# Optimization experiments

Measured on AMD Instinct MI355X. Metric: run time of the kernel, lower is better.

## Reference

```python
import jax, jax.numpy as jnp
import numpy as np


def setup_inputs() -> dict:
    key = jax.random.key(0)
    k1, k2, k3 = jax.random.split(key, 3)
    B, Cin, H, W = 64, 16, 256, 256
    Cout, K = 64, 3
    x = jax.random.normal(k1, (B, Cin, H, W), dtype=jnp.float32)
    # PyTorch Conv2d init scale ~ 1/sqrt(fan_in)
    fan_in = Cin * K * K
    conv_weight = jax.random.normal(k2, (Cout, Cin, K, K), dtype=jnp.float32) / np.sqrt(fan_in)
    conv_bias = jax.random.normal(k3, (Cout,), dtype=jnp.float32) / np.sqrt(fan_in)
    return {"x": x, "conv_weight": conv_weight, "conv_bias": conv_bias}


def reference(x, conv_weight, conv_bias):
    # Conv2d: stride=1, padding=0 (VALID), dilation=1, groups=1
    y = jax.lax.conv_general_dilated(
        x, conv_weight,
        window_strides=(1, 1),
        padding="VALID",
        dimension_numbers=("NCHW", "OIHW", "NCHW"),
    ) + conv_bias[None, :, None, None]          # [B, Cout, 254, 254]
    m = jnp.min(y, axis=1, keepdims=True)        # [B, 1, 254, 254] min over channels
    return jnp.tanh(jnp.tanh(m))                 # double tanh
```

## Files before the change

### kernel.cpp

```cpp
#include <hip/hip_runtime.h>
#include <math.h>

#define CIN   16
#define COUT  64
#define H     256
#define W     256
#define OH    254
#define OW    254
#define NTAP  9
#define HWSZ  (H * W)
#define TOR   8
#define TIR   10
#define SROW  264
#define BUFS  (TIR * SROW)
#define NTILE 16

typedef _Float16 f16x8  __attribute__((ext_vector_type(8)));
typedef float    f32x16 __attribute__((ext_vector_type(16)));

__global__ void wpack_kernel(const float* __restrict__ w, _Float16* __restrict__ wpk) {
    int idx = blockIdx.x * 256 + threadIdx.x;
    if (idx >= NTAP * 2 * 64 * 8) return;
    int e = idx & 7, l = (idx >> 3) & 63, m = (idx >> 9) & 1, t = idx >> 10;
    int co  = (l & 31) + 32 * m;
    int cin = 8 * (l >> 5) + e;
    wpk[idx] = (_Float16)w[((co * CIN + cin) * 3 + t / 3) * 3 + (t % 3)];
}

__device__ __forceinline__ float tanh_fast(float v) {
    float e = __expf(2.0f * v);
    return 1.0f - 2.0f * __builtin_amdgcn_rcpf(e + 1.0f);
}
__device__ __forceinline__ float min3f(float a, float b, float c) {
    return fminf(fminf(a, b), c);
}

__global__ __launch_bounds__(512, 2) void conv_mfma_kernel(
        const float* __restrict__ x, const f16x8* __restrict__ wpk,
        const float* __restrict__ bias, float* __restrict__ out) {
    __shared__ f16x8 xs[2][BUFS];

    const int tid  = threadIdx.x;
    const int lane = tid & 63;

    int bid = blockIdx.x;
    int nb  = (bid & 7) * 32 + (bid >> 3);
    const int img  = nb >> 2;
    const int half = (nb >> 1) & 1;
    const int col  = nb & 1;
    const int base = col * 124;
    const int P0   = col * 128;
    const int R0   = half * 128;

    const float* xb = x + (size_t)img * CIN * HWSZ;

    f16x8 wreg[NTAP][2];
#pragma unroll
    for (int t = 0; t < NTAP; ++t)
#pragma unroll
        for (int m = 0; m < 2; ++m)
            wreg[t][m] = wpk[(t * 2 + m) * 64 + lane];

    int row_[3], g_[3], pp_[3];
#pragma unroll
    for (int k = 0; k < 3; ++k) {
        int u = tid + 512 * k;
        row_[k] = u / 132;
        int rem = u - 132 * row_[k];
        g_[k]  = (rem >= 66) ? 1 : 0;
        pp_[k] = rem - 66 * g_[k];
    }
    const bool act2 = (tid < 296);

#define SLOADK(k, rbase, vv)                                                    \
    {                                                                           \
        int grow = (rbase) + row_[k]; if (grow > 255) grow = 255;               \
        const float* gp = xb + (size_t)g_[k] * 8 * HWSZ + (size_t)grow * W      \
                             + base + 2 * pp_[k];                               \
        _Pragma("unroll")                                                       \
        for (int c = 0; c < 8; ++c) vv[c] = *(const float2*)(gp + (size_t)c * HWSZ); \
    }

#define SWRITEK(k, bufp, vv)                                                    \
    {                                                                           \
        f16x8 q0, q1;                                                           \
        _Pragma("unroll")                                                       \
        for (int c = 0; c < 8; ++c) { q0[c] = (_Float16)vv[c].x;                \
                                      q1[c] = (_Float16)vv[c].y; }              \
        int sl_ = row_[k] * SROW + g_[k] * 132 + 2 * pp_[k];                    \
        (bufp)[sl_]     = q0;                                                   \
        (bufp)[sl_ + 1] = q1;                                                   \
    }

    {
        float2 v0[8], v1[8], v2[8];
        SLOADK(0, R0, v0)
        SLOADK(1, R0, v1)
        if (act2) SLOADK(2, R0, v2)
        SWRITEK(0, xs[0], v0)
        SWRITEK(1, xs[0], v1)
        if (act2) SWRITEK(2, xs[0], v2)
    }

    const int wave = tid >> 6;
    const int pr   = wave >> 2;
    const int sl4  = wave & 3;
    const int l31  = lane & 31;
    const int g2   = lane >> 5;

    int roff[3];
#pragma unroll
    for (int kw = 0; kw < 3; ++kw) {
        int lp = (col ? 4 : 0) + 32 * sl4 + l31 + kw;
        if (lp > 131) lp = 131;
        roff[kw] = g2 * 132 + lp;
    }

    f32x16 cbias[2];
#pragma unroll
    for (int m = 0; m < 2; ++m)
#pragma unroll
        for (int r = 0; r < 16; ++r)
            cbias[m][r] = bias[(r & 3) + 8 * (r >> 2) + 4 * g2 + 32 * m];

    __syncthreads();

    float2 vA[8], vB[8], vC[8];
    int cur = 0;

#pragma unroll 1
    for (int t = 0; t < NTILE; ++t) {
        const int r0 = R0 + t * TOR;
        const bool pf = (t + 1 < NTILE);

        if (pf) {
            const int rn = r0 + TOR;
            SLOADK(0, rn, vA)
            SLOADK(1, rn, vB)
            if (act2) SLOADK(2, rn, vC)
        }
        __builtin_amdgcn_sched_barrier(0);

        const f16x8* bufc = &xs[cur][0];

#pragma unroll
        for (int i = 0; i < 2; ++i) {
            f32x16 acc[2][2];
#pragma unroll
            for (int dd = 0; dd < 4; ++dd) {
                const f16x8* xr = bufc + (4 * i + 2 * pr + dd) * SROW;
                f16x8 f0 = xr[roff[0]];
                f16x8 f1 = xr[roff[1]];
                f16x8 f2 = xr[roff[2]];
#pragma unroll
                for (int ro = 0; ro < 2; ++ro) {
                    const int kh = dd - ro;
                    if (kh < 0 || kh > 2) continue;
#pragma unroll
                    for (int m = 0; m < 2; ++m) {
                        if (kh == 0)
                            acc[ro][m] = __builtin_amdgcn_mfma_f32_32x32x16_f16(wreg[0][m], f0, cbias[m], 0, 0, 0);
                        else
                            acc[ro][m] = __builtin_amdgcn_mfma_f32_32x32x16_f16(wreg[kh * 3][m], f0, acc[ro][m], 0, 0, 0);
                        acc[ro][m] = __builtin_amdgcn_mfma_f32_32x32x16_f16(wreg[kh * 3 + 1][m], f1, acc[ro][m], 0, 0, 0);
                        acc[ro][m] = __builtin_amdgcn_mfma_f32_32x32x16_f16(wreg[kh * 3 + 2][m], f2, acc[ro][m], 0, 0, 0);
                    }
                }
            }
#pragma unroll
            for (int ro = 0; ro < 2; ++ro) {
                const int oh = r0 + 4 * i + 2 * pr + ro;
                float mn = fminf(acc[ro][0][0], acc[ro][1][0]);
#pragma unroll
                for (int q = 1; q < 16; ++q)
                    mn = min3f(acc[ro][0][q], acc[ro][1][q], mn);
                mn = fminf(mn, __shfl_xor(mn, 32));
                float t2 = tanh_fast(tanh_fast(mn));
                const int px = P0 + 32 * sl4 + l31;
                if (g2 == 0 && px < OW && oh < OH)
                    out[((size_t)img * OH + oh) * OW + px] = t2;
            }
        }
        __builtin_amdgcn_sched_barrier(0);

        if (pf) {
            f16x8* bufn = &xs[cur ^ 1][0];
            SWRITEK(0, bufn, vA)
            SWRITEK(1, bufn, vB)
            if (act2) SWRITEK(2, bufn, vC)
        }
        __syncthreads();
        cur ^= 1;
    }
}

extern "C" void kernel_launch(void* const* d_in, const int* in_sizes, int n_in,
                              void* d_out, int out_size, void* d_ws, size_t ws_size,
                              hipStream_t stream) {
    const float* x    = (const float*)d_in[0];
    const float* w    = (const float*)d_in[1];
    const float* bias = (const float*)d_in[2];
    float* out = (float*)d_out;
    _Float16* wpk = (_Float16*)d_ws;

    wpack_kernel<<<36, 256, 0, stream>>>(w, wpk);
    conv_mfma_kernel<<<256, 512, 0, stream>>>(x, (const f16x8*)wpk, bias, out);
}
```

Measured before the change: 110.1 us.

## Switch conv to 18-row LDS ring buffer with narrower 64-column tiles

Replaces the double-buffered 10-row tile (which reloads the 2-row halo each step) with an 18-row circular LDS ring, so only 8 new rows are fetched per iteration and halo rows are reused. Blocks shrink to 256 threads covering 64-column strips, launched as 512 blocks, and the bias is staged in LDS and read per tile instead of held in registers. The prefetch is issued after the LDS write for the next tile, which gives the global load a full iteration of compute to hide behind. Narrower strips add more horizontal halo overhead and the ring needs modular slot arithmetic.

```diff
diff --git a/kernel.cpp b/kernel.cpp
--- a/kernel.cpp
+++ b/kernel.cpp
@@ -9,11 +9,8 @@
 #define OW    254
 #define NTAP  9
 #define HWSZ  (H * W)
-#define TOR   8
-#define TIR   10
-#define SROW  264
-#define BUFS  (TIR * SROW)
-#define NTILE 16
+#define RING  18
+#define SROW  136
 
 typedef _Float16 f16x8  __attribute__((ext_vector_type(8)));
 typedef float    f32x16 __attribute__((ext_vector_type(16)));
@@ -35,22 +32,24 @@
     return fminf(fminf(a, b), c);
 }
 
-__global__ __launch_bounds__(512, 2) void conv_mfma_kernel(
+__global__ __launch_bounds__(256, 2) void conv_mfma_kernel(
         const float* __restrict__ x, const f16x8* __restrict__ wpk,
         const float* __restrict__ bias, float* __restrict__ out) {
-    __shared__ f16x8 xs[2][BUFS];
+    __shared__ f16x8 ring[RING * SROW];
+    __shared__ float bias_lds[64];
 
     const int tid  = threadIdx.x;
     const int lane = tid & 63;
 
     int bid = blockIdx.x;
-    int nb  = (bid & 7) * 32 + (bid >> 3);
-    const int img  = nb >> 2;
-    const int half = (nb >> 1) & 1;
-    const int col  = nb & 1;
-    const int base = col * 124;
-    const int P0   = col * 128;
-    const int R0   = half * 128;
+    int nb  = (bid & 7) * 64 + (bid >> 3);
+    const int img  = nb >> 3;
+    const int rem  = nb & 7;
+    const int colb = rem & 3;
+    const int half = rem >> 2;
+    const int base = 64 * colb;
+    const int R0   = 128 * half;
+    const int S0   = half ? 2 : 0;
 
     const float* xb = x + (size_t)img * CIN * HWSZ;
 
@@ -61,136 +60,148 @@
         for (int m = 0; m < 2; ++m)
             wreg[t][m] = wpk[(t * 2 + m) * 64 + lane];
 
-    int row_[3], g_[3], pp_[3];
+    if (tid < 64) {
+        int q = tid & 15, m = (tid >> 4) & 1, g = tid >> 5;
+        bias_lds[tid] = bias[(q & 3) + 8 * (q >> 2) + 4 * g + 32 * m];
+    }
+
+    int r8[3], gq[3], gx[3], wof[3];
 #pragma unroll
     for (int k = 0; k < 3; ++k) {
-        int u = tid + 512 * k;
-        row_[k] = u / 132;
-        int rem = u - 132 * row_[k];
-        g_[k]  = (rem >= 66) ? 1 : 0;
-        pp_[k] = rem - 66 * g_[k];
-    }
-    const bool act2 = (tid < 296);
-
-#define SLOADK(k, rbase, vv)                                                    \
+        int u  = tid + 256 * k;
+        r8[k]  = u / 68;
+        int r2 = u - 68 * r8[k];
+        int g  = (r2 >= 34) ? 1 : 0;
+        int p  = r2 - 34 * g;
+        int px = base + 2 * p; if (px > 254) px = 254;
+        gq[k]  = g;
+        gx[k]  = px;
+        wof[k] = g * 68 + 2 * p;
+    }
+    const bool act2 = (tid < 32);
+
+    float2 vA[8], vB[8], vC[8];
+
+#define PLOADK(k, rowAbs, vv)                                                   \
     {                                                                           \
-        int grow = (rbase) + row_[k]; if (grow > 255) grow = 255;               \
-        const float* gp = xb + (size_t)g_[k] * 8 * HWSZ + (size_t)grow * W      \
-                             + base + 2 * pp_[k];                               \
+        int gr = (rowAbs); if (gr > 255) gr = 255;                              \
+        const float* gp = xb + (size_t)(8 * gq[k]) * HWSZ + (size_t)gr * W + gx[k]; \
         _Pragma("unroll")                                                       \
-        for (int c = 0; c < 8; ++c) vv[c] = *(const float2*)(gp + (size_t)c * HWSZ); \
-    }
-
-#define SWRITEK(k, bufp, vv)                                                    \
+        for (int cc = 0; cc < 8; ++cc) vv[cc] = *(const float2*)(gp + (size_t)cc * HWSZ); \
+    }
+
+#define PWRITEK(k, slot, vv)                                                    \
     {                                                                           \
         f16x8 q0, q1;                                                           \
         _Pragma("unroll")                                                       \
-        for (int c = 0; c < 8; ++c) { q0[c] = (_Float16)vv[c].x;                \
-                                      q1[c] = (_Float16)vv[c].y; }              \
-        int sl_ = row_[k] * SROW + g_[k] * 132 + 2 * pp_[k];                    \
-        (bufp)[sl_]     = q0;                                                   \
-        (bufp)[sl_ + 1] = q1;                                                   \
-    }
-
-    {
-        float2 v0[8], v1[8], v2[8];
-        SLOADK(0, R0, v0)
-        SLOADK(1, R0, v1)
-        if (act2) SLOADK(2, R0, v2)
-        SWRITEK(0, xs[0], v0)
-        SWRITEK(1, xs[0], v1)
-        if (act2) SWRITEK(2, xs[0], v2)
-    }
-
-    const int wave = tid >> 6;
-    const int pr   = wave >> 2;
-    const int sl4  = wave & 3;
-    const int l31  = lane & 31;
-    const int g2   = lane >> 5;
-
-    int roff[3];
-#pragma unroll
-    for (int kw = 0; kw < 3; ++kw) {
-        int lp = (col ? 4 : 0) + 32 * sl4 + l31 + kw;
-        if (lp > 131) lp = 131;
-        roff[kw] = g2 * 132 + lp;
-    }
-
-    f32x16 cbias[2];
-#pragma unroll
-    for (int m = 0; m < 2; ++m)
-#pragma unroll
-        for (int r = 0; r < 16; ++r)
-            cbias[m][r] = bias[(r & 3) + 8 * (r >> 2) + 4 * g2 + 32 * m];
-
+        for (int cc = 0; cc < 8; ++cc) { q0[cc] = (_Float16)vv[cc].x;           \
+                                         q1[cc] = (_Float16)vv[cc].y; }         \
+        const int ad = (slot) * SROW + wof[k];                                  \
+        ring[ad]     = q0;                                                      \
+        ring[ad + 1] = q1;                                                      \
+    }
+
+#pragma unroll
+    for (int k = 0; k < 3; ++k) {
+        int u = tid + 256 * k;
+        if (k == 2 && tid >= 168) break;
+        int r10 = u / 68;
+        int r2  = u - 68 * r10;
+        int g   = (r2 >= 34) ? 1 : 0;
+        int p   = r2 - 34 * g;
+        int px  = base + 2 * p; if (px > 254) px = 254;
+        const float* gp = xb + (size_t)(8 * g) * HWSZ + (size_t)(R0 + r10) * W + px;
+        float2 vm[8];
+#pragma unroll
+        for (int cc = 0; cc < 8; ++cc) vm[cc] = *(const float2*)(gp + (size_t)cc * HWSZ);
+        f16x8 q0, q1;
+#pragma unroll
+        for (int cc = 0; cc < 8; ++cc) { q0[cc] = (_Float16)vm[cc].x;
+                                         q1[cc] = (_Float16)vm[cc].y; }
+        const int ad = (S0 + r10) * SROW + g * 68 + 2 * p;
+        ring[ad]     = q0;
+        ring[ad + 1] = q1;
+    }
+
+    PLOADK(0, R0 + 10 + r8[0], vA)
+    PLOADK(1, R0 + 10 + r8[1], vB)
+    if (act2) PLOADK(2, R0 + 10 + r8[2], vC)
     __syncthreads();
 
-    float2 vA[8], vB[8], vC[8];
-    int cur = 0;
+    const int wv  = tid >> 6;
+    const int s   = wv & 1;
+    const int rg  = wv >> 1;
+    const int l31 = lane & 31;
+    const int g2  = lane >> 5;
+    const int foff = g2 * 68 + 32 * s + l31;
+    const int opx  = base + 32 * s + l31;
+    const size_t obase = (size_t)img * OH * OW;
+    const f32x16* bp = (const f32x16*)(bias_lds + g2 * 32);
+
+    int slot0 = S0;
 
 #pragma unroll 1
-    for (int t = 0; t < NTILE; ++t) {
-        const int r0 = R0 + t * TOR;
-        const bool pf = (t + 1 < NTILE);
-
-        if (pf) {
-            const int rn = r0 + TOR;
-            SLOADK(0, rn, vA)
-            SLOADK(1, rn, vB)
-            if (act2) SLOADK(2, rn, vC)
-        }
-        __builtin_amdgcn_sched_barrier(0);
-
-        const f16x8* bufc = &xs[cur][0];
-
-#pragma unroll
-        for (int i = 0; i < 2; ++i) {
+    for (int t = 0; t < 16; ++t) {
+        const int row0 = R0 + 8 * t;
+
+#pragma unroll
+        for (int c = 0; c < 2; ++c) {
+            const int rowoff = 4 * rg + 2 * c;
+            f32x16 cb0 = bp[0], cb1 = bp[1];
             f32x16 acc[2][2];
 #pragma unroll
             for (int dd = 0; dd < 4; ++dd) {
-                const f16x8* xr = bufc + (4 * i + 2 * pr + dd) * SROW;
-                f16x8 f0 = xr[roff[0]];
-                f16x8 f1 = xr[roff[1]];
-                f16x8 f2 = xr[roff[2]];
-#pragma unroll
-                for (int ro = 0; ro < 2; ++ro) {
-                    const int kh = dd - ro;
-                    if (kh < 0 || kh > 2) continue;
-#pragma unroll
-                    for (int m = 0; m < 2; ++m) {
-                        if (kh == 0)
-                            acc[ro][m] = __builtin_amdgcn_mfma_f32_32x32x16_f16(wreg[0][m], f0, cbias[m], 0, 0, 0);
-                        else
-                            acc[ro][m] = __builtin_amdgcn_mfma_f32_32x32x16_f16(wreg[kh * 3][m], f0, acc[ro][m], 0, 0, 0);
-                        acc[ro][m] = __builtin_amdgcn_mfma_f32_32x32x16_f16(wreg[kh * 3 + 1][m], f1, acc[ro][m], 0, 0, 0);
-                        acc[ro][m] = __builtin_amdgcn_mfma_f32_32x32x16_f16(wreg[kh * 3 + 2][m], f2, acc[ro][m], 0, 0, 0);
+                int sl = slot0 + rowoff + dd; if (sl >= RING) sl -= RING;
+                const f16x8* rp = ring + sl * SROW + foff;
+                f16x8 f0 = rp[0], f1 = rp[1], f2 = rp[2];
+#pragma unroll
+                for (int kw = 0; kw < 3; ++kw) {
+                    f16x8 ff = (kw == 0) ? f0 : (kw == 1) ? f1 : f2;
+#pragma unroll
+                    for (int ro = 0; ro < 2; ++ro) {
+                        const int kh = dd - ro;
+                        if (kh < 0 || kh > 2) continue;
+#pragma unroll
+                        for (int m = 0; m < 2; ++m) {
+                            const f32x16& cin_ = (kh == 0 && kw == 0)
+                                               ? (m == 0 ? cb0 : cb1) : acc[ro][m];
+                            acc[ro][m] = __builtin_amdgcn_mfma_f32_32x32x16_f16(
+                                wreg[kh * 3 + kw][m], ff, cin_, 0, 0, 0);
+                        }
                     }
                 }
             }
 #pragma unroll
             for (int ro = 0; ro < 2; ++ro) {
-                const int oh = r0 + 4 * i + 2 * pr + ro;
                 float mn = fminf(acc[ro][0][0], acc[ro][1][0]);
 #pragma unroll
                 for (int q = 1; q < 16; ++q)
                     mn = min3f(acc[ro][0][q], acc[ro][1][q], mn);
                 mn = fminf(mn, __shfl_xor(mn, 32));
                 float t2 = tanh_fast(tanh_fast(mn));
-                const int px = P0 + 32 * sl4 + l31;
-                if (g2 == 0 && px < OW && oh < OH)
-                    out[((size_t)img * OH + oh) * OW + px] = t2;
+                const int oh = row0 + rowoff + ro;
+                if (g2 == 0 && oh < OH && opx < OW)
+                    out[obase + (size_t)oh * OW + opx] = t2;
             }
         }
-        __builtin_amdgcn_sched_barrier(0);
-
-        if (pf) {
-            f16x8* bufn = &xs[cur ^ 1][0];
-            SWRITEK(0, bufn, vA)
-            SWRITEK(1, bufn, vB)
-            if (act2) SWRITEK(2, bufn, vC)
+
+        if (t <= 14) {
+            int sl0 = slot0 + 10 + r8[0]; if (sl0 >= RING) sl0 -= RING;
+            int sl1 = slot0 + 10 + r8[1]; if (sl1 >= RING) sl1 -= RING;
+            PWRITEK(0, sl0, vA)
+            PWRITEK(1, sl1, vB)
+            if (act2) {
+                int sl2 = slot0 + 10 + r8[2]; if (sl2 >= RING) sl2 -= RING;
+                PWRITEK(2, sl2, vC)
+            }
+        }
+        if (t <= 13) {
+            PLOADK(0, row0 + 18 + r8[0], vA)
+            PLOADK(1, row0 + 18 + r8[1], vB)
+            if (act2) PLOADK(2, row0 + 18 + r8[2], vC)
         }
         __syncthreads();
-        cur ^= 1;
+        slot0 += 8; if (slot0 >= RING) slot0 -= RING;
     }
 }
 
@@ -204,5 +215,5 @@
     _Float16* wpk = (_Float16*)d_ws;
 
     wpack_kernel<<<36, 256, 0, stream>>>(w, wpk);
-    conv_mfma_kernel<<<256, 512, 0, stream>>>(x, (const f16x8*)wpk, bias, out);
-}
+    conv_mfma_kernel<<<512, 256, 0, stream>>>(x, (const f16x8*)wpk, bias, out);
+}
```

After: 91.64 us. 1.2x faster.
